# Kernel tuning notes

Hardware: AMD Instinct MI355X
Metric: run time of the kernel (lower is better)

The kernel has to match this reference:

```python
import jax, jax.numpy as jnp
import numpy as np

B, T, F = 64, 96, 32          # batch, window_size, num_features
H_ENC, H_DEC = 128, 128       # encoder / decoder hidden sizes


def _lstm_cell(x, h, c, k, r, b):
    # Keras LSTMCell math: gates ordered i, f, g(candidate), o
    z = x @ k + h @ r + b
    i, f, g, o = jnp.split(z, 4, axis=-1)
    i = jax.nn.sigmoid(i)
    f = jax.nn.sigmoid(f)
    g = jnp.tanh(g)
    o = jax.nn.sigmoid(o)
    c_new = f * c + i * g
    h_new = o * jnp.tanh(c_new)
    return h_new, c_new


def setup_inputs() -> dict:
    key = jax.random.key(0)
    ks = jax.random.split(key, 20)
    s = 0.05
    d = {
        "inputs": jax.random.normal(ks[0], (B, T, F), jnp.float32),
        # encoder LSTMCell (input dim = F)
        "enc_k": jax.random.normal(ks[1], (F, 4 * H_ENC), jnp.float32) * s,
        "enc_r": jax.random.normal(ks[2], (H_ENC, 4 * H_ENC), jnp.float32) * s,
        "enc_b": jnp.zeros((4 * H_ENC,), jnp.float32),
        # encoder attention MLP: in = 2*H_ENC + T -> H_ENC -> 1
        "ae_w1": jax.random.normal(ks[3], (2 * H_ENC + T, H_ENC), jnp.float32) * s,
        "ae_b1": jnp.zeros((H_ENC,), jnp.float32),
        "ae_w2": jax.random.normal(ks[4], (H_ENC, 1), jnp.float32) * s,
        "ae_b2": jnp.zeros((1,), jnp.float32),
        # decoder LSTMCell (input dim = H_DEC, the fc output)
        "dec_k": jax.random.normal(ks[5], (H_DEC, 4 * H_DEC), jnp.float32) * s,
        "dec_r": jax.random.normal(ks[6], (H_DEC, 4 * H_DEC), jnp.float32) * s,
        "dec_b": jnp.zeros((4 * H_DEC,), jnp.float32),
        # decoder attention MLP: in = 2*H_DEC + H_ENC -> H_ENC -> 1
        "ad_w1": jax.random.normal(ks[7], (2 * H_DEC + H_ENC, H_ENC), jnp.float32) * s,
        "ad_b1": jnp.zeros((H_ENC,), jnp.float32),
        "ad_w2": jax.random.normal(ks[8], (H_ENC, 1), jnp.float32) * s,
        "ad_b2": jnp.zeros((1,), jnp.float32),
        # fc: (context H_ENC + y_prev 1) -> H_DEC
        "fc_w": jax.random.normal(ks[9], (H_ENC + 1, H_DEC), jnp.float32) * s,
        "fc_b": jnp.zeros((H_DEC,), jnp.float32),
        # fc_final: (d_n H_DEC + context H_ENC) -> F
        "ff_w": jax.random.normal(ks[10], (H_DEC + H_ENC, F), jnp.float32) * s,
        "ff_b": jnp.zeros((F,), jnp.float32),
    }
    return d


def reference(inputs, enc_k, enc_r, enc_b, ae_w1, ae_b1, ae_w2, ae_b2,
              dec_k, dec_r, dec_b, ad_w1, ad_b1, ad_w2, ad_b2,
              fc_w, fc_b, ff_w, ff_b):
    b, t, f = inputs.shape
    h_enc = enc_r.shape[0]
    h_dec = dec_r.shape[0]
    x_perm = jnp.transpose(inputs, (0, 2, 1))  # [B, F, T] (constant over time)

    # ---------------- encoder: input-attention LSTM over time ----------------
    def enc_step(carry, x_t):
        h, s = carry  # each [B, H_enc]
        hb = jnp.broadcast_to(h[:, None, :], (b, f, h_enc))
        sb = jnp.broadcast_to(s[:, None, :], (b, f, h_enc))
        cat = jnp.concatenate([hb, sb, x_perm], axis=2)       # [B, F, 2H+T]
        e = jnp.tanh(cat @ ae_w1 + ae_b1) @ ae_w2 + ae_b2     # [B, F, 1]
        alpha = jax.nn.softmax(e[..., 0], axis=1)             # [B, F]
        x_tilde = alpha * x_t                                 # [B, F]
        h, s = _lstm_cell(x_tilde, h, s, enc_k, enc_r, enc_b)
        return (h, s), h

    init = (jnp.zeros((b, h_enc), inputs.dtype), jnp.zeros((b, h_enc), inputs.dtype))
    _, h_all = jax.lax.scan(enc_step, init, jnp.transpose(inputs, (1, 0, 2)))
    x_encoded = jnp.transpose(h_all, (1, 0, 2))               # [B, T, H_enc]

    # ---------------- decoder: temporal-attention LSTM over time -------------
    y_prev = inputs[:, :, -1]                                 # [B, T]

    def dec_step(carry, y_t):
        d, c, _ = carry
        db = jnp.broadcast_to(d[:, None, :], (b, t, h_dec))
        cb = jnp.broadcast_to(c[:, None, :], (b, t, h_dec))
        cat = jnp.concatenate([db, cb, x_encoded], axis=2)    # [B, T, 2Hd+He]
        e = jnp.tanh(cat @ ad_w1 + ad_b1) @ ad_w2 + ad_b2     # [B, T, 1]
        beta = jax.nn.softmax(e[..., 0], axis=1)              # [B, T]
        ctx = jnp.einsum("bt,bth->bh", beta, x_encoded)       # [B, H_enc]
        y_tilde = jnp.concatenate([ctx, y_t[:, None]], axis=1) @ fc_w + fc_b
        d, c = _lstm_cell(y_tilde, d, c, dec_k, dec_r, dec_b)
        return (d, c, ctx), None

    init_d = (jnp.zeros((b, h_dec), inputs.dtype),
              jnp.zeros((b, h_dec), inputs.dtype),
              jnp.zeros((b, h_enc), inputs.dtype))
    (d_n, _, ctx), _ = jax.lax.scan(dec_step, init_d, jnp.transpose(y_prev, (1, 0)))

    y_pred = jnp.concatenate([d_n, ctx], axis=1) @ ff_w + ff_b  # [B, F]
    return y_pred[:, None, :]                                   # [B, 1, F]
```

## Files before the change

kernel.cpp:

```cpp
#include <hip/hip_runtime.h>

#define TT 96
#define FF 32
#define HH 128
#define G4 512
#define LOG2E 1.4426950408889634f

typedef _Float16 h2 __attribute__((ext_vector_type(2)));

__device__ __forceinline__ float fexp2(float x){ return __builtin_amdgcn_exp2f(x); }
__device__ __forceinline__ float frcp(float x){ return __builtin_amdgcn_rcpf(x); }
__device__ __forceinline__ float fsigmoid(float x){ return frcp(1.0f + fexp2(-LOG2E*x)); }
__device__ __forceinline__ float ftanh(float x){
    float u = fexp2(2.0f*LOG2E*x);
    return 1.0f - 2.0f*frcp(1.0f + u);
}
__device__ __forceinline__ h2 pk(float a, float b){
    h2 r; r.x = (_Float16)a; r.y = (_Float16)b; return r;
}
__device__ __forceinline__ unsigned pku(float a, float b){
    return __builtin_bit_cast(unsigned, pk(a, b));
}
__device__ __forceinline__ h2 u2h(unsigned v){ return __builtin_bit_cast(h2, v); }
__device__ __forceinline__ float fdot2(h2 a, h2 b, float c){
#if __has_builtin(__builtin_amdgcn_fdot2)
    return __builtin_amdgcn_fdot2(a, b, c, false);
#else
    return c + (float)a.x*(float)b.x + (float)a.y*(float)b.y;
#endif
}

__global__ __launch_bounds__(1024, 1)
void k_enc(const float* __restrict__ inputs,
           const float* __restrict__ enc_k,
           const float* __restrict__ enc_r,
           const float* __restrict__ enc_b,
           const float* __restrict__ ae_w1,
           const float* __restrict__ ae_b1,
           const float* __restrict__ ae_w2,
           const float* __restrict__ ad_w1,
           const float* __restrict__ fc_w,
           const float* __restrict__ fc_b,
           const float* __restrict__ dec_k,
           const float* __restrict__ dec_b,
           h2* __restrict__ Gp,
           float* __restrict__ gy,
           float* __restrict__ gb,
           float* __restrict__ ws_xenc,
           float* __restrict__ ws_xept){
    if (blockIdx.x >= 64){
        int blk = blockIdx.x - 64, tid = threadIdx.x;
        if (tid >= 256) return;
        int u0 = tid, u1 = tid + 256;
        if (blk < 16){
            float a0[8], a1[8];
            #pragma unroll
            for (int r = 0; r < 8; ++r){ a0[r] = 0.f; a1[r] = 0.f; }
            for (int m = 0; m < 128; ++m){
                float d0 = dec_k[m*G4 + u0], d1 = dec_k[m*G4 + u1];
                #pragma unroll
                for (int r = 0; r < 8; ++r){
                    float w = fc_w[(blk*8 + r)*HH + m];
                    a0[r] += w * d0; a1[r] += w * d1;
                }
            }
            #pragma unroll
            for (int c = 0; c < 4; ++c){
                Gp[(blk*G4 + u0)*4 + c] = pk(a0[2*c], a0[2*c+1]);
                Gp[(blk*G4 + u1)*4 + c] = pk(a1[2*c], a1[2*c+1]);
            }
        } else if (blk == 16){
            float a0 = 0.f, a1 = 0.f;
            for (int m = 0; m < 128; ++m){
                float w = fc_w[128*HH + m];
                a0 += w * dec_k[m*G4 + u0]; a1 += w * dec_k[m*G4 + u1];
            }
            gy[u0] = a0; gy[u1] = a1;
        } else {
            float a0 = 0.f, a1 = 0.f;
            for (int m = 0; m < 128; ++m){
                float w = fc_b[m];
                a0 += w * dec_k[m*G4 + u0]; a1 += w * dec_k[m*G4 + u1];
            }
            gb[u0] = a0 + dec_b[u0]; gb[u1] = a1 + dec_b[u1];
        }
        return;
    }

    extern __shared__ float lds[];
    uint4* KLH4 = (uint4*)lds;
    float* XPJT = lds + 8192;
    float* XIN  = lds + 12416;
    float* HST  = lds + 15488;
    float* PP   = lds + 15744;
    float* PPZ  = lds + 16768;
    float* PE   = lds + 17792;
    float* W2E  = lds + 17920;
    float* AB1E = lds + 18048;
    h2*    HSP  = (h2*)(lds + 18176);
    h2*    XTP  = (h2*)(lds + 18240);
    _Float16* XEF = (_Float16*)(lds + 18248);

    const int b = blockIdx.x, tid = threadIdx.x;
    const int u = tid & 511, hf = tid >> 9;
    const int j7 = tid & 127, g8 = tid >> 7;
    const float* xin_g = inputs + b*TT*FF;

    for (int i = tid; i < TT*FF; i += 1024) XIN[i] = xin_g[i];
    for (int i = tid; i < 2048; i += 1024){
        int f8 = i >> 9, uu = i & 511;
        uint4 q;
        q.x = pku(enc_k[(f8*8+0)*G4+uu], enc_k[(f8*8+1)*G4+uu]);
        q.y = pku(enc_k[(f8*8+2)*G4+uu], enc_k[(f8*8+3)*G4+uu]);
        q.z = pku(enc_k[(f8*8+4)*G4+uu], enc_k[(f8*8+5)*G4+uu]);
        q.w = pku(enc_k[(f8*8+6)*G4+uu], enc_k[(f8*8+7)*G4+uu]);
        KLH4[i] = q;
    }
    if (tid < 128){ W2E[tid] = ae_w2[tid]; AB1E[tid] = ae_b1[tid]; HSP[tid] = pk(0.f, 0.f); }
    if (tid < 256) HST[tid] = 0.f;

    h2 rp_e[32];
    #pragma unroll
    for (int i = 0; i < 32; ++i)
        rp_e[i] = pk(enc_r[(hf*64 + 2*i)*G4 + u], enc_r[(hf*64 + 2*i+1)*G4 + u]);

    uint4 wae[4];
    #pragma unroll
    for (int i4 = 0; i4 < 4; ++i4){
        int r0 = (g8*4 + i4)*8;
        wae[i4].x = pku(ae_w1[(r0+0)*HH + j7], ae_w1[(r0+1)*HH + j7]);
        wae[i4].y = pku(ae_w1[(r0+2)*HH + j7], ae_w1[(r0+3)*HH + j7]);
        wae[i4].z = pku(ae_w1[(r0+4)*HH + j7], ae_w1[(r0+5)*HH + j7]);
        wae[i4].w = pku(ae_w1[(r0+6)*HH + j7], ae_w1[(r0+7)*HH + j7]);
    }

    const float eb = (hf == 0) ? enc_b[u] : 0.f;
    __syncthreads();

    {
        int j = tid & 127, fh = tid >> 7;
        float a0=0.f, a1=0.f, a2=0.f, a3=0.f;
        for (int t = 0; t < TT; ++t){
            float w = ae_w1[(256 + t)*HH + j];
            const float* xr = &XIN[t*FF + fh*4];
            a0 += xr[0]*w; a1 += xr[1]*w; a2 += xr[2]*w; a3 += xr[3]*w;
        }
        XPJT[j*33 + fh*4 + 0] = a0;
        XPJT[j*33 + fh*4 + 1] = a1;
        XPJT[j*33 + fh*4 + 2] = a2;
        XPJT[j*33 + fh*4 + 3] = a3;
    }
    __syncthreads();

    const int f5 = tid & 31, jg5 = tid >> 5;
    float er_e[4], sumw2e = 0.f;
    #pragma unroll
    for (int i = 0; i < 4; ++i){
        er_e[i] = fexp2(2.0f*LOG2E * XPJT[(jg5*4 + i)*33 + f5]);
        sumw2e += W2E[jg5*4 + i];
    }

    const uint4* HSP4 = (const uint4*)HSP;
    const uint4* XTP4 = (const uint4*)XTP;

    for (int t = 0; t < TT; ++t){
        float z = eb;
        {
            float a0 = 0.f, a1 = 0.f;
            #pragma unroll
            for (int i4 = 0; i4 < 4; ++i4){
                uint4 q  = HSP4[g8*4 + i4];
                uint4 wv = wae[i4];
                a0 = fdot2(u2h(q.x), u2h(wv.x), a0);
                a1 = fdot2(u2h(q.y), u2h(wv.y), a1);
                a0 = fdot2(u2h(q.z), u2h(wv.z), a0);
                a1 = fdot2(u2h(q.w), u2h(wv.w), a1);
            }
            PP[tid] = a0 + a1;
        }
        if (tid < 128){
            float z2 = 0.f;
            #pragma unroll
            for (int i4 = 0; i4 < 8; ++i4){
                uint4 q = HSP4[hf*8 + i4];
                z  = fdot2(u2h(q.x), rp_e[i4*4+0], z);
                z2 = fdot2(u2h(q.y), rp_e[i4*4+1], z2);
                z  = fdot2(u2h(q.z), rp_e[i4*4+2], z);
                z2 = fdot2(u2h(q.w), rp_e[i4*4+3], z2);
            }
            z += z2;
        }
        __syncthreads();
        if (tid < 128){
            float s = AB1E[tid];
            #pragma unroll
            for (int g = 0; g < 8; ++g) s += PP[tid + 128*g];
            PE[tid] = fexp2(2.0f*LOG2E * s);
        } else {
            float z2 = 0.f;
            #pragma unroll
            for (int i4 = 0; i4 < 8; ++i4){
                uint4 q = HSP4[hf*8 + i4];
                z  = fdot2(u2h(q.x), rp_e[i4*4+0], z);
                z2 = fdot2(u2h(q.y), rp_e[i4*4+1], z2);
                z  = fdot2(u2h(q.z), rp_e[i4*4+2], z);
                z2 = fdot2(u2h(q.w), rp_e[i4*4+3], z2);
            }
            z += z2;
        }
        __syncthreads();
        {
            float acc2 = 0.f;
            #pragma unroll
            for (int i = 0; i < 4; ++i){
                float uu = PE[jg5*4 + i];
                float w  = W2E[jg5*4 + i];
                acc2 += w * frcp(fmaf(er_e[i], uu, 1.0f));
            }
            PP[tid] = sumw2e - 2.0f*acc2;
        }
        __syncthreads();
        if (tid < 64){
            int f = tid & 31, hh = tid >> 5;
            float e = 0.f;
            #pragma unroll
            for (int g = 0; g < 16; ++g) e += PP[(hh*16 + g)*32 + f];
            e += __shfl_xor(e, 32, 64);
            float p = fexp2(e * LOG2E);
            float ss = p;
            #pragma unroll
            for (int d = 16; d; d >>= 1) ss += __shfl_xor(ss, d, 32);
            if (tid < 32){
                float xt = p * frcp(ss) * XIN[t*FF + tid];
                float xt2 = __shfl_xor(xt, 1);
                if (!(tid & 1)) XTP[tid >> 1] = pk(xt, xt2);
            }
        }
        __syncthreads();
        {
            float z2 = 0.f;
            #pragma unroll
            for (int c = 0; c < 2; ++c){
                int f8 = hf*2 + c;
                uint4 kq = KLH4[f8*512 + u];
                uint4 xq = XTP4[f8];
                z  = fdot2(u2h(kq.x), u2h(xq.x), z);
                z2 = fdot2(u2h(kq.y), u2h(xq.y), z2);
                z  = fdot2(u2h(kq.z), u2h(xq.z), z);
                z2 = fdot2(u2h(kq.w), u2h(xq.w), z2);
            }
            PPZ[hf*512 + u] = z + z2;
        }
        __syncthreads();
        if (tid < 128){
            int j = tid;
            float zi = PPZ[j]       + PPZ[512 + j];
            float zf = PPZ[128 + j] + PPZ[640 + j];
            float zg = PPZ[256 + j] + PPZ[768 + j];
            float zo = PPZ[384 + j] + PPZ[896 + j];
            float iv = fsigmoid(zi);
            float fv = fsigmoid(zf);
            float gv = ftanh(zg);
            float ov = fsigmoid(zo);
            float cn = fv * HST[128 + j] + iv * gv;
            float hn = ov * ftanh(cn);
            HST[128 + j] = cn;
            HST[j] = hn;
            ws_xenc[(b*TT + t)*HH + j] = hn;
            XEF[t*HH + j] = (_Float16)hn;
            float hn2 = __shfl_xor(hn, 1);
            float cn2 = __shfl_xor(cn, 1);
            if (!(j & 1)){
                HSP[j >> 1]        = pk(hn, hn2);
                HSP[64 + (j >> 1)] = pk(cn, cn2);
            }
        }
        __syncthreads();
    }

    {
        int j = tid & 127, th = tid >> 7;
        float acc[12];
        #pragma unroll
        for (int i = 0; i < 12; ++i) acc[i] = 0.f;
        for (int k = 0; k < 128; ++k){
            float w = ad_w1[(256 + k)*HH + j];
            #pragma unroll
            for (int i = 0; i < 12; ++i)
                acc[i] += (float)XEF[(th*12 + i)*HH + k] * w;
        }
        #pragma unroll
        for (int i = 0; i < 12; ++i)
            ws_xept[(b*HH + j)*TT + th*12 + i] = acc[i];
    }
}

__global__ __launch_bounds__(1024, 1)
void k_dec(const float* __restrict__ inputs,
           const float* __restrict__ dec_r,
           const float* __restrict__ ad_w1,
           const float* __restrict__ ad_b1,
           const float* __restrict__ ad_w2,
           const float* __restrict__ ff_w,
           const float* __restrict__ ff_b,
           const h2* __restrict__ Gp,
           const float* __restrict__ gy,
           const float* __restrict__ gb,
           const float* __restrict__ ws_xenc,
           const float* __restrict__ ws_xept,
           float* __restrict__ out){
    extern __shared__ float lds[];
    uint4* XE4 = (uint4*)lds;
    uint4* WDC4= (uint4*)(lds + 6144);
    float* PP  = lds + 22528;
    float* PPZ = lds + 23552;
    float* PPA = lds + 24576;
    float* APJ = lds + 25600;
    float* DST = lds + 25728;
    float* CTX = lds + 25984;
    float* W2L = lds + 26112;
    float* YV  = lds + 26240;
    float* SCAL= lds + 26336;
    h2*    DCP = (h2*)(lds + 26344);
    h2*    CXP = (h2*)(lds + 26408);
    h2*    BEP = (h2*)(lds + 26440);

    const int b = blockIdx.x, tid = threadIdx.x;
    const int u = tid & 511, hf = tid >> 9;
    const int j = tid & 127, og = tid >> 7;

    {
        const float* xe_g = ws_xenc + b*TT*HH;
        for (int i = tid; i < 12*HH; i += 1024){
            int t8 = i >> 7, k = i & 127;
            uint4 qq;
            qq.x = pku(xe_g[(t8*8 + 0)*HH + k], xe_g[(t8*8 + 1)*HH + k]);
            qq.y = pku(xe_g[(t8*8 + 2)*HH + k], xe_g[(t8*8 + 3)*HH + k]);
            qq.z = pku(xe_g[(t8*8 + 4)*HH + k], xe_g[(t8*8 + 5)*HH + k]);
            qq.w = pku(xe_g[(t8*8 + 6)*HH + k], xe_g[(t8*8 + 7)*HH + k]);
            XE4[i] = qq;
        }
    }
    for (int i = tid; i < 4096; i += 1024){
        int jj = i & 127, i4g = i >> 7;
        int kbase = (i4g >> 2)*32 + (i4g & 3)*8;
        uint4 wv;
        wv.x = pku(ad_w1[(kbase+0)*HH + jj], ad_w1[(kbase+1)*HH + jj]);
        wv.y = pku(ad_w1[(kbase+2)*HH + jj], ad_w1[(kbase+3)*HH + jj]);
        wv.z = pku(ad_w1[(kbase+4)*HH + jj], ad_w1[(kbase+5)*HH + jj]);
        wv.w = pku(ad_w1[(kbase+6)*HH + jj], ad_w1[(kbase+7)*HH + jj]);
        WDC4[i] = wv;
    }
    if (tid < TT) YV[tid] = inputs[b*TT*FF + tid*FF + (FF-1)];
    if (tid < 128) DCP[tid] = pk(0.f, 0.f);
    if (tid < 256) DST[tid] = 0.f;

    h2 rp[32];
    #pragma unroll
    for (int i = 0; i < 32; ++i)
        rp[i] = pk(dec_r[(hf*64 + 2*i)*G4 + u], dec_r[(hf*64 + 2*i+1)*G4 + u]);

    uint4 Greg[8];
    {
        const uint4* GQ = (const uint4*)Gp;
        #pragma unroll
        for (int g = 0; g < 8; ++g) Greg[g] = GQ[(hf*8 + g)*G4 + u];
    }

    float erw[16], iw[16], sumw2 = 0.f;
    {
        const float* xp_g = ws_xept + (b*HH + og*16)*TT + j;
        #pragma unroll
        for (int i = 0; i < 16; ++i){
            float w2v = ad_w2[og*16 + i];
            float ivv = 1.0f / w2v;
            iw[i] = ivv;
            sumw2 += w2v;
            float xp = (j < TT) ? xp_g[i*TT] : 0.f;
            erw[i] = fexp2(2.0f*LOG2E * xp) * ivv;
        }
    }

    const float gbr = gb[u], gyr = gy[u];
    const float ab1 = (tid < 128) ? ad_b1[tid] : 0.f;
    __syncthreads();

    const uint4* DCP4 = (const uint4*)DCP;
    const uint4* CXP4 = (const uint4*)CXP;
    const uint4* BEP4 = (const uint4*)BEP;

    for (int t = 0; t < TT; ++t){
        float z = (hf == 0) ? (gbr + YV[t]*gyr) : 0.f;
        {
            float s0 = 0.f, s1 = 0.f;
            #pragma unroll
            for (int i = 0; i < 4; ++i){
                uint4 dq = DCP4[og*4 + i];
                uint4 wv = WDC4[(og*4 + i)*128 + j];
                s0 = fdot2(u2h(dq.x), u2h(wv.x), s0);
                s1 = fdot2(u2h(dq.y), u2h(wv.y), s1);
                s0 = fdot2(u2h(dq.z), u2h(wv.z), s0);
                s1 = fdot2(u2h(dq.w), u2h(wv.w), s1);
            }
            PPA[og*128 + j] = s0 + s1;
        }
        if (tid < 128){
            float z2 = 0.f;
            #pragma unroll
            for (int i4 = 0; i4 < 8; ++i4){
                uint4 q = DCP4[hf*8 + i4];
                z  = fdot2(u2h(q.x), rp[i4*4+0], z);
                z2 = fdot2(u2h(q.y), rp[i4*4+1], z2);
                z  = fdot2(u2h(q.z), rp[i4*4+2], z);
                z2 = fdot2(u2h(q.w), rp[i4*4+3], z2);
            }
            z += z2;
        }
        __syncthreads();
        if (tid < 128){
            float s = ab1;
            #pragma unroll
            for (int g = 0; g < 8; ++g) s += PPA[tid + 128*g];
            APJ[tid] = fexp2(2.0f*LOG2E * s);
        } else {
            float z2 = 0.f;
            #pragma unroll
            for (int i4 = 0; i4 < 8; ++i4){
                uint4 q = DCP4[hf*8 + i4];
                z  = fdot2(u2h(q.x), rp[i4*4+0], z);
                z2 = fdot2(u2h(q.y), rp[i4*4+1], z2);
                z  = fdot2(u2h(q.z), rp[i4*4+2], z);
                z2 = fdot2(u2h(q.w), rp[i4*4+3], z2);
            }
            z += z2;
        }
        __syncthreads();
        {
            float acc = 0.f;
            if (j < TT){
                float acc2 = 0.f;
                #pragma unroll
                for (int q4 = 0; q4 < 4; ++q4){
                    float4 uj = *(const float4*)&APJ[og*16 + q4*4];
                    acc2 += frcp(fmaf(erw[q4*4+0], uj.x, iw[q4*4+0]));
                    acc2 += frcp(fmaf(erw[q4*4+1], uj.y, iw[q4*4+1]));
                    acc2 += frcp(fmaf(erw[q4*4+2], uj.z, iw[q4*4+2]));
                    acc2 += frcp(fmaf(erw[q4*4+3], uj.w, iw[q4*4+3]));
                }
                acc = sumw2 - 2.0f*acc2;
            }
            PP[tid] = acc;
        }
        __syncthreads();
        if (tid < 64){
            float ea = 0.f;
            #pragma unroll
            for (int g = 0; g < 8; ++g) ea += PP[tid + 128*g];
            float pa = fexp2(ea * LOG2E);
            float pb = 0.f;
            if (tid < 32){
                float ebv = 0.f;
                #pragma unroll
                for (int g = 0; g < 8; ++g) ebv += PP[64 + tid + 128*g];
                pb = fexp2(ebv * LOG2E);
            }
            float ss = pa + pb;
            #pragma unroll
            for (int d = 32; d; d >>= 1) ss += __shfl_xor(ss, d, 64);
            float pa2 = __shfl_xor(pa, 1);
            float pb2 = __shfl_xor(pb, 1);
            if (!(tid & 1)){
                BEP[tid >> 1] = pk(pa, pa2);
                if (tid < 32) BEP[32 + (tid >> 1)] = pk(pb, pb2);
            }
            if (tid == 0) SCAL[0] = frcp(ss);
        }
        __syncthreads();
        if (tid < 128){
            float s0 = 0.f, s1 = 0.f;
            #pragma unroll
            for (int t8 = 0; t8 < 12; t8 += 2){
                uint4 xq0 = XE4[t8*HH + tid],     bb0 = BEP4[t8];
                uint4 xq1 = XE4[(t8+1)*HH + tid], bb1 = BEP4[t8+1];
                s0 = fdot2(u2h(xq0.x), u2h(bb0.x), s0);
                s1 = fdot2(u2h(xq0.y), u2h(bb0.y), s1);
                s0 = fdot2(u2h(xq0.z), u2h(bb0.z), s0);
                s1 = fdot2(u2h(xq0.w), u2h(bb0.w), s1);
                s0 = fdot2(u2h(xq1.x), u2h(bb1.x), s0);
                s1 = fdot2(u2h(xq1.y), u2h(bb1.y), s1);
                s0 = fdot2(u2h(xq1.z), u2h(bb1.z), s0);
                s1 = fdot2(u2h(xq1.w), u2h(bb1.w), s1);
            }
            float cv = (s0 + s1) * SCAL[0];
            CTX[tid] = cv;
            float cv2 = __shfl_xor(cv, 1);
            if (!(tid & 1)) CXP[tid >> 1] = pk(cv, cv2);
        }
        __syncthreads();
        {
            float z2 = 0.f;
            #pragma unroll
            for (int gi = 0; gi < 8; ++gi){
                uint4 q  = Greg[gi];
                uint4 cc = CXP4[hf*8 + gi];
                z  = fdot2(u2h(q.x), u2h(cc.x), z);
                z2 = fdot2(u2h(q.y), u2h(cc.y), z2);
                z  = fdot2(u2h(q.z), u2h(cc.z), z);
                z2 = fdot2(u2h(q.w), u2h(cc.w), z2);
            }
            PPZ[hf*512 + u] = z + z2;
        }
        __syncthreads();
        if (tid < 128){
            int jj = tid;
            float zi = PPZ[jj]       + PPZ[512 + jj];
            float zf = PPZ[128 + jj] + PPZ[640 + jj];
            float zg = PPZ[256 + jj] + PPZ[768 + jj];
            float zo = PPZ[384 + jj] + PPZ[896 + jj];
            float iv = fsigmoid(zi);
            float fv = fsigmoid(zf);
            float gv = ftanh(zg);
            float ov = fsigmoid(zo);
            float cn = fv * DST[128 + jj] + iv * gv;
            float hn = ov * ftanh(cn);
            DST[128 + jj] = cn;
            DST[jj] = hn;
            float hn2 = __shfl_xor(hn, 1);
            float cn2 = __shfl_xor(cn, 1);
            if (!(jj & 1)){
                DCP[jj >> 1]        = pk(hn, hn2);
                DCP[64 + (jj >> 1)] = pk(cn, cn2);
            }
        }
        __syncthreads();
    }

    {
        int jp = tid & 31, sg = tid >> 5;
        float a = 0.f;
        #pragma unroll
        for (int kk = 0; kk < 8; ++kk){
            int k = sg*8 + kk;
            float val = (k < 128) ? DST[k] : CTX[k - 128];
            a += val * ff_w[k*FF + jp];
        }
        PP[sg*32 + jp] = a;
    }
    __syncthreads();
    if (tid < 32){
        float o = ff_b[tid];
        #pragma unroll
        for (int s = 0; s < 32; ++s) o += PP[s*32 + tid];
        out[b*FF + tid] = o;
    }
}

extern "C" void kernel_launch(void* const* d_in, const int* in_sizes, int n_in,
                              void* d_out, int out_size, void* d_ws, size_t ws_size,
                              hipStream_t stream) {
    const float* inputs = (const float*)d_in[0];
    const float* enc_k  = (const float*)d_in[1];
    const float* enc_r  = (const float*)d_in[2];
    const float* enc_b  = (const float*)d_in[3];
    const float* ae_w1  = (const float*)d_in[4];
    const float* ae_b1  = (const float*)d_in[5];
    const float* ae_w2  = (const float*)d_in[6];
    const float* dec_k  = (const float*)d_in[8];
    const float* dec_r  = (const float*)d_in[9];
    const float* dec_b  = (const float*)d_in[10];
    const float* ad_w1  = (const float*)d_in[11];
    const float* ad_b1  = (const float*)d_in[12];
    const float* ad_w2  = (const float*)d_in[13];
    const float* fc_w   = (const float*)d_in[15];
    const float* fc_b   = (const float*)d_in[16];
    const float* ff_w   = (const float*)d_in[17];
    const float* ff_b   = (const float*)d_in[18];

    float* ws      = (float*)d_ws;
    float* ws_xenc = ws;
    float* ws_xept = ws + 786432;
    h2*    Gp      = (h2*)(ws + 1572864);
    float* gy      = ws + 1605632;
    float* gb      = ws + 1606144;

    hipFuncSetAttribute((const void*)k_enc, hipFuncAttributeMaxDynamicSharedMemorySize, 97568);
    hipFuncSetAttribute((const void*)k_dec, hipFuncAttributeMaxDynamicSharedMemorySize, 105888);

    k_enc<<<82, 1024, 97568, stream>>>(inputs, enc_k, enc_r, enc_b, ae_w1, ae_b1, ae_w2,
                                       ad_w1, fc_w, fc_b, dec_k, dec_b, Gp, gy, gb,
                                       ws_xenc, ws_xept);
    k_dec<<<64, 1024, 105888, stream>>>(inputs, dec_r, ad_w1, ad_b1, ad_w2, ff_w, ff_b,
                                        Gp, gy, gb, ws_xenc, ws_xept, (float*)d_out);
}
```

Measured before the change: 660.6 us.

## Replace LDS attention-score reductions with wave shuffles and drop a barrier per step

```diff
diff --git a/kernel.cpp b/kernel.cpp
--- a/kernel.cpp
+++ b/kernel.cpp
@@ -100,6 +100,7 @@
     h2*    HSP  = (h2*)(lds + 18176);
     h2*    XTP  = (h2*)(lds + 18240);
     _Float16* XEF = (_Float16*)(lds + 18248);
+    float* WSUME= lds + 24392;
 
     const int b = blockIdx.x, tid = threadIdx.x;
     const int u = tid & 511, hf = tid >> 9;
@@ -152,12 +153,13 @@
     }
     __syncthreads();
 
-    const int f5 = tid & 31, jg5 = tid >> 5;
+    const int l6e = tid & 63, wv6e = tid >> 6;
+    const int fq = wv6e*2 + (l6e & 1), jgq = l6e >> 1;
     float er_e[4], sumw2e = 0.f;
     #pragma unroll
     for (int i = 0; i < 4; ++i){
-        er_e[i] = fexp2(2.0f*LOG2E * XPJT[(jg5*4 + i)*33 + f5]);
-        sumw2e += W2E[jg5*4 + i];
+        er_e[i] = fexp2(2.0f*LOG2E * XPJT[(jgq*4 + i)*33 + fq]);
+        sumw2e += W2E[jgq*4 + i];
     }
 
     const uint4* HSP4 = (const uint4*)HSP;
@@ -213,43 +215,45 @@
             float acc2 = 0.f;
             #pragma unroll
             for (int i = 0; i < 4; ++i){
-                float uu = PE[jg5*4 + i];
-                float w  = W2E[jg5*4 + i];
-                acc2 += w * frcp(fmaf(er_e[i], uu, 1.0f));
-            }
-            PP[tid] = sumw2e - 2.0f*acc2;
-        }
-        __syncthreads();
-        if (tid < 64){
-            int f = tid & 31, hh = tid >> 5;
-            float e = 0.f;
-            #pragma unroll
-            for (int g = 0; g < 16; ++g) e += PP[(hh*16 + g)*32 + f];
-            e += __shfl_xor(e, 32, 64);
-            float p = fexp2(e * LOG2E);
-            float ss = p;
-            #pragma unroll
-            for (int d = 16; d; d >>= 1) ss += __shfl_xor(ss, d, 32);
-            if (tid < 32){
-                float xt = p * frcp(ss) * XIN[t*FF + tid];
-                float xt2 = __shfl_xor(xt, 1);
-                if (!(tid & 1)) XTP[tid >> 1] = pk(xt, xt2);
+                float uu = PE[jgq*4 + i];
+                float wq = W2E[jgq*4 + i];
+                acc2 += wq * frcp(fmaf(er_e[i], uu, 1.0f));
+            }
+            float part = sumw2e - 2.0f*acc2;
+            part += __shfl_xor(part, 2);
+            part += __shfl_xor(part, 4);
+            part += __shfl_xor(part, 8);
+            part += __shfl_xor(part, 16);
+            part += __shfl_xor(part, 32);
+            float p = fexp2(part * LOG2E);
+            float xt = p * XIN[t*FF + fq];
+            float xt2 = __shfl_xor(xt, 1);
+            float pss = (jgq == 0) ? p : 0.f;
+            pss += __shfl_xor(pss, 1);
+            if (l6e == 0){
+                XTP[wv6e] = pk(xt, xt2);
+                WSUME[wv6e] = pss;
             }
         }
         __syncthreads();
         {
-            float z2 = 0.f;
+            float ssn = 0.f;
+            #pragma unroll
+            for (int g = 0; g < 16; ++g) ssn += WSUME[g];
+            float rs = frcp(ssn);
+            float zk = 0.f, zk2 = 0.f;
             #pragma unroll
             for (int c = 0; c < 2; ++c){
                 int f8 = hf*2 + c;
                 uint4 kq = KLH4[f8*512 + u];
                 uint4 xq = XTP4[f8];
-                z  = fdot2(u2h(kq.x), u2h(xq.x), z);
-                z2 = fdot2(u2h(kq.y), u2h(xq.y), z2);
-                z  = fdot2(u2h(kq.z), u2h(xq.z), z);
-                z2 = fdot2(u2h(kq.w), u2h(xq.w), z2);
-            }
-            PPZ[hf*512 + u] = z + z2;
+                zk  = fdot2(u2h(kq.x), u2h(xq.x), zk);
+                zk2 = fdot2(u2h(kq.y), u2h(xq.y), zk2);
+                zk  = fdot2(u2h(kq.z), u2h(xq.z), zk);
+                zk2 = fdot2(u2h(kq.w), u2h(xq.w), zk2);
+            }
+            z += (zk + zk2) * rs;
+            PPZ[hf*512 + u] = z;
         }
         __syncthreads();
         if (tid < 128){
@@ -318,7 +322,7 @@
     float* APJ = lds + 25600;
     float* DST = lds + 25728;
     float* CTX = lds + 25984;
-    float* W2L = lds + 26112;
+    float* WSUM= lds + 26112;
     float* YV  = lds + 26240;
     float* SCAL= lds + 26336;
     h2*    DCP = (h2*)(lds + 26344);
@@ -367,16 +371,20 @@
         for (int g = 0; g < 8; ++g) Greg[g] = GQ[(hf*8 + g)*G4 + u];
     }
 
+    const int l6 = tid & 63, wv6 = tid >> 6;
+    const int ogn = l6 & 7, tpl = l6 >> 3;
+    const int tpn = wv6*6 + tpl;
+    const bool act = (tpl < 6);
     float erw[16], iw[16], sumw2 = 0.f;
     {
-        const float* xp_g = ws_xept + (b*HH + og*16)*TT + j;
+        const float* xp_g = ws_xept + (b*HH + ogn*16)*TT + tpn;
         #pragma unroll
         for (int i = 0; i < 16; ++i){
-            float w2v = ad_w2[og*16 + i];
+            float w2v = ad_w2[ogn*16 + i];
             float ivv = 1.0f / w2v;
             iw[i] = ivv;
             sumw2 += w2v;
-            float xp = (j < TT) ? xp_g[i*TT] : 0.f;
+            float xp = act ? xp_g[i*TT] : 0.f;
             erw[i] = fexp2(2.0f*LOG2E * xp) * ivv;
         }
     }
@@ -436,47 +444,38 @@
         }
         __syncthreads();
         {
-            float acc = 0.f;
-            if (j < TT){
+            float part = 0.f;
+            if (act){
                 float acc2 = 0.f;
                 #pragma unroll
                 for (int q4 = 0; q4 < 4; ++q4){
-                    float4 uj = *(const float4*)&APJ[og*16 + q4*4];
+                    float4 uj = *(const float4*)&APJ[ogn*16 + q4*4];
                     acc2 += frcp(fmaf(erw[q4*4+0], uj.x, iw[q4*4+0]));
                     acc2 += frcp(fmaf(erw[q4*4+1], uj.y, iw[q4*4+1]));
                     acc2 += frcp(fmaf(erw[q4*4+2], uj.z, iw[q4*4+2]));
                     acc2 += frcp(fmaf(erw[q4*4+3], uj.w, iw[q4*4+3]));
                 }
-                acc = sumw2 - 2.0f*acc2;
-            }
-            PP[tid] = acc;
-        }
-        __syncthreads();
-        if (tid < 64){
-            float ea = 0.f;
-            #pragma unroll
-            for (int g = 0; g < 8; ++g) ea += PP[tid + 128*g];
-            float pa = fexp2(ea * LOG2E);
-            float pb = 0.f;
-            if (tid < 32){
-                float ebv = 0.f;
-                #pragma unroll
-                for (int g = 0; g < 8; ++g) ebv += PP[64 + tid + 128*g];
-                pb = fexp2(ebv * LOG2E);
-            }
-            float ss = pa + pb;
-            #pragma unroll
-            for (int d = 32; d; d >>= 1) ss += __shfl_xor(ss, d, 64);
-            float pa2 = __shfl_xor(pa, 1);
-            float pb2 = __shfl_xor(pb, 1);
-            if (!(tid & 1)){
-                BEP[tid >> 1] = pk(pa, pa2);
-                if (tid < 32) BEP[32 + (tid >> 1)] = pk(pb, pb2);
-            }
-            if (tid == 0) SCAL[0] = frcp(ss);
-        }
-        __syncthreads();
-        if (tid < 128){
+                part = sumw2 - 2.0f*acc2;
+            }
+            part += __shfl_xor(part, 1);
+            part += __shfl_xor(part, 2);
+            part += __shfl_xor(part, 4);
+            float p = fexp2(part * LOG2E);
+            float p2 = __shfl_xor(p, 8);
+            if (act && ogn == 0 && !(tpl & 1))
+                BEP[wv6*3 + (tpl >> 1)] = pk(p, p2);
+            float pss = (act && ogn == 0) ? p : 0.f;
+            pss += __shfl_xor(pss, 8);
+            pss += __shfl_xor(pss, 16);
+            pss += __shfl_xor(pss, 32);
+            if (l6 == 0) WSUM[wv6] = pss;
+        }
+        __syncthreads();
+        if (tid < 128){
+            float ssn = 0.f;
+            #pragma unroll
+            for (int g = 0; g < 16; ++g) ssn += WSUM[g];
+            float rs = frcp(ssn);
             float s0 = 0.f, s1 = 0.f;
             #pragma unroll
             for (int t8 = 0; t8 < 12; t8 += 2){
@@ -491,7 +490,7 @@
                 s0 = fdot2(u2h(xq1.z), u2h(bb1.z), s0);
                 s1 = fdot2(u2h(xq1.w), u2h(bb1.w), s1);
             }
-            float cv = (s0 + s1) * SCAL[0];
+            float cv = (s0 + s1) * rs;
             CTX[tid] = cv;
             float cv2 = __shfl_xor(cv, 1);
             if (!(tid & 1)) CXP[tid >> 1] = pk(cv, cv2);
@@ -583,10 +582,10 @@
     float* gy      = ws + 1605632;
     float* gb      = ws + 1606144;
 
-    hipFuncSetAttribute((const void*)k_enc, hipFuncAttributeMaxDynamicSharedMemorySize, 97568);
+    hipFuncSetAttribute((const void*)k_enc, hipFuncAttributeMaxDynamicSharedMemorySize, 97632);
     hipFuncSetAttribute((const void*)k_dec, hipFuncAttributeMaxDynamicSharedMemorySize, 105888);
 
-    k_enc<<<82, 1024, 97568, stream>>>(inputs, enc_k, enc_r, enc_b, ae_w1, ae_b1, ae_w2,
+    k_enc<<<82, 1024, 97632, stream>>>(inputs, enc_k, enc_r, enc_b, ae_w1, ae_b1, ae_w2,
                                        ad_w1, fc_w, fc_b, dec_k, dec_b, Gp, gy, gb,
                                        ws_xenc, ws_xept);
     k_dec<<<64, 1024, 105888, stream>>>(inputs, dec_r, ad_w1, ad_b1, ad_w2, ff_w, ff_b,
```

Measured after the change: 679.7 us. 2.9% more time.

## Remap decoder attention scoring to warp-local reduction, removing a barrier per step

Applied to the files above, without the earlier changes.

```diff
diff --git a/kernel.cpp b/kernel.cpp
--- a/kernel.cpp
+++ b/kernel.cpp
@@ -315,15 +315,14 @@
     float* PP  = lds + 22528;
     float* PPZ = lds + 23552;
     float* PPA = lds + 24576;
-    float* APJ = lds + 25600;
-    float* DST = lds + 25728;
-    float* CTX = lds + 25984;
-    float* W2L = lds + 26112;
-    float* YV  = lds + 26240;
-    float* SCAL= lds + 26336;
-    h2*    DCP = (h2*)(lds + 26344);
-    h2*    CXP = (h2*)(lds + 26408);
-    h2*    BEP = (h2*)(lds + 26440);
+    float* APJP= lds + 25600;
+    float* DST = lds + 25760;
+    float* CTX = lds + 26016;
+    float* WSUM= lds + 26144;
+    float* YV  = lds + 26160;
+    h2*    DCP = (h2*)(lds + 26256);
+    h2*    CXP = (h2*)(lds + 26384);
+    h2*    BEP = (h2*)(lds + 26448);
 
     const int b = blockIdx.x, tid = threadIdx.x;
     const int u = tid & 511, hf = tid >> 9;
@@ -367,16 +366,20 @@
         for (int g = 0; g < 8; ++g) Greg[g] = GQ[(hf*8 + g)*G4 + u];
     }
 
+    const int l6 = tid & 63, wv6 = tid >> 6;
+    const int ogn = l6 & 7, tpl = l6 >> 3;
+    const int tpn = wv6*6 + tpl;
+    const bool act = (tpl < 6);
     float erw[16], iw[16], sumw2 = 0.f;
     {
-        const float* xp_g = ws_xept + (b*HH + og*16)*TT + j;
+        const float* xp_g = ws_xept + (b*HH + ogn*16)*TT + tpn;
         #pragma unroll
         for (int i = 0; i < 16; ++i){
-            float w2v = ad_w2[og*16 + i];
+            float w2v = ad_w2[ogn*16 + i];
             float ivv = 1.0f / w2v;
             iw[i] = ivv;
             sumw2 += w2v;
-            float xp = (j < TT) ? xp_g[i*TT] : 0.f;
+            float xp = act ? xp_g[i*TT] : 0.f;
             erw[i] = fexp2(2.0f*LOG2E * xp) * ivv;
         }
     }
@@ -421,7 +424,7 @@
             float s = ab1;
             #pragma unroll
             for (int g = 0; g < 8; ++g) s += PPA[tid + 128*g];
-            APJ[tid] = fexp2(2.0f*LOG2E * s);
+            APJP[(tid >> 4)*20 + (tid & 15)] = fexp2(2.0f*LOG2E * s);
         } else {
             float z2 = 0.f;
             #pragma unroll
@@ -436,47 +439,38 @@
         }
         __syncthreads();
         {
-            float acc = 0.f;
-            if (j < TT){
+            float part = 0.f;
+            if (act){
                 float acc2 = 0.f;
                 #pragma unroll
                 for (int q4 = 0; q4 < 4; ++q4){
-                    float4 uj = *(const float4*)&APJ[og*16 + q4*4];
+                    float4 uj = *(const float4*)&APJP[ogn*20 + q4*4];
                     acc2 += frcp(fmaf(erw[q4*4+0], uj.x, iw[q4*4+0]));
                     acc2 += frcp(fmaf(erw[q4*4+1], uj.y, iw[q4*4+1]));
                     acc2 += frcp(fmaf(erw[q4*4+2], uj.z, iw[q4*4+2]));
                     acc2 += frcp(fmaf(erw[q4*4+3], uj.w, iw[q4*4+3]));
                 }
-                acc = sumw2 - 2.0f*acc2;
-            }
-            PP[tid] = acc;
-        }
-        __syncthreads();
-        if (tid < 64){
-            float ea = 0.f;
-            #pragma unroll
-            for (int g = 0; g < 8; ++g) ea += PP[tid + 128*g];
-            float pa = fexp2(ea * LOG2E);
-            float pb = 0.f;
-            if (tid < 32){
-                float ebv = 0.f;
-                #pragma unroll
-                for (int g = 0; g < 8; ++g) ebv += PP[64 + tid + 128*g];
-                pb = fexp2(ebv * LOG2E);
-            }
-            float ss = pa + pb;
-            #pragma unroll
-            for (int d = 32; d; d >>= 1) ss += __shfl_xor(ss, d, 64);
-            float pa2 = __shfl_xor(pa, 1);
-            float pb2 = __shfl_xor(pb, 1);
-            if (!(tid & 1)){
-                BEP[tid >> 1] = pk(pa, pa2);
-                if (tid < 32) BEP[32 + (tid >> 1)] = pk(pb, pb2);
-            }
-            if (tid == 0) SCAL[0] = frcp(ss);
-        }
-        __syncthreads();
-        if (tid < 128){
+                part = sumw2 - 2.0f*acc2;
+            }
+            part += __shfl_xor(part, 1);
+            part += __shfl_xor(part, 2);
+            part += __shfl_xor(part, 4);
+            float p = fexp2(part * LOG2E);
+            float p2 = __shfl_xor(p, 8);
+            if (act && ogn == 0 && !(tpl & 1))
+                BEP[wv6*3 + (tpl >> 1)] = pk(p, p2);
+            float pss = (act && ogn == 0) ? p : 0.f;
+            pss += __shfl_xor(pss, 8);
+            pss += __shfl_xor(pss, 16);
+            pss += __shfl_xor(pss, 32);
+            if (l6 == 0) WSUM[wv6] = pss;
+        }
+        __syncthreads();
+        if (tid < 128){
+            float ssn = 0.f;
+            #pragma unroll
+            for (int g = 0; g < 16; ++g) ssn += WSUM[g];
+            float rs = frcp(ssn);
             float s0 = 0.f, s1 = 0.f;
             #pragma unroll
             for (int t8 = 0; t8 < 12; t8 += 2){
@@ -491,7 +485,7 @@
                 s0 = fdot2(u2h(xq1.z), u2h(bb1.z), s0);
                 s1 = fdot2(u2h(xq1.w), u2h(bb1.w), s1);
             }
-            float cv = (s0 + s1) * SCAL[0];
+            float cv = (s0 + s1) * rs;
             CTX[tid] = cv;
             float cv2 = __shfl_xor(cv, 1);
             if (!(tid & 1)) CXP[tid >> 1] = pk(cv, cv2);
@@ -584,11 +578,11 @@
     float* gb      = ws + 1606144;
 
     hipFuncSetAttribute((const void*)k_enc, hipFuncAttributeMaxDynamicSharedMemorySize, 97568);
-    hipFuncSetAttribute((const void*)k_dec, hipFuncAttributeMaxDynamicSharedMemorySize, 105888);
+    hipFuncSetAttribute((const void*)k_dec, hipFuncAttributeMaxDynamicSharedMemorySize, 106048);
 
     k_enc<<<82, 1024, 97568, stream>>>(inputs, enc_k, enc_r, enc_b, ae_w1, ae_b1, ae_w2,
                                        ad_w1, fc_w, fc_b, dec_k, dec_b, Gp, gy, gb,
                                        ws_xenc, ws_xept);
-    k_dec<<<64, 1024, 105888, stream>>>(inputs, dec_r, ad_w1, ad_b1, ad_w2, ff_w, ff_b,
+    k_dec<<<64, 1024, 106048, stream>>>(inputs, dec_r, ad_w1, ad_b1, ad_w2, ff_w, ff_b,
                                         Gp, gy, gb, ws_xenc, ws_xept, (float*)d_out);
 }
```

New measurement: 652.1 us (median of 2 runs). Within noise of the previous version (-1.3%).
